# Kernel optimization log

Measured on AMD Instinct MI355X. Metric: run time of the kernel, lower is better.

Reference implementation:

```python
import jax, jax.numpy as jnp
import numpy as np

N_NODES = 50000
N_EDGES = 500000
D_IN = 128
D_OUT = 128


def setup_inputs() -> dict:
    key = jax.random.key(0)
    k1, k2, k3 = jax.random.split(key, 3)
    x = jax.random.normal(k1, (N_NODES, D_IN), dtype=jnp.float32)
    edge_index = jax.random.randint(k2, (2, N_EDGES), 0, N_NODES, dtype=jnp.int64)
    W = jax.random.normal(k3, (D_IN, D_OUT), dtype=jnp.float32) / np.sqrt(D_IN)
    b = jnp.zeros((D_OUT,), dtype=jnp.float32)
    return {"x": x, "edge_index": edge_index, "W": W, "b": b}


def reference(x, edge_index, W, b):
    # GCNConv (PyG defaults): add self-loops, symmetric normalization, linear, bias.
    N = x.shape[0]
    loop = jnp.arange(N, dtype=edge_index.dtype)
    src = jnp.concatenate([edge_index[0], loop])  # message source (row)
    dst = jnp.concatenate([edge_index[1], loop])  # aggregation target (col)
    # degree of target nodes (with self-loops)
    deg = jax.ops.segment_sum(jnp.ones_like(dst, dtype=x.dtype), dst, num_segments=N)
    dinv = jnp.where(deg > 0, jax.lax.rsqrt(deg), 0.0)
    norm = dinv[src] * dinv[dst]  # [E+N]
    xw = x @ W                    # [N, D_OUT] transform before propagate
    msg = xw[src] * norm[:, None] # [E+N, D_OUT] gather + normalize
    out = jax.ops.segment_sum(msg, dst, num_segments=N) + b
    # relu; dropout is identity at inference
    return jax.nn.relu(out)
```

## Files before the change

### kernel.cpp

```cpp
#include <hip/hip_runtime.h>

#define NN 50000
#define NE 500000
#define DD 128
#define CAP 64
#define SPILLCAP 4096

typedef __attribute__((ext_vector_type(8))) short bf16x8;
typedef __attribute__((ext_vector_type(4))) float f32x4;


__device__ __forceinline__ unsigned int bf16pair(float a, float b) {
    unsigned int ua = __float_as_uint(a);
    ua = (ua + 0x7FFFu + ((ua >> 16) & 1u)) >> 16;
    unsigned int ub = __float_as_uint(b);
    ub = (ub + 0x7FFFu + ((ub >> 16) & 1u)) >> 16;
    return ua | (ub << 16);
}
__device__ __forceinline__ float bflo(unsigned int u) { return __uint_as_float(u << 16); }
__device__ __forceinline__ float bfhi(unsigned int u) { return __uint_as_float(u & 0xFFFF0000u); }

__global__ void k_init(const float* __restrict__ W, unsigned int* __restrict__ Wf,
                       int* __restrict__ cnt, int* __restrict__ spill_n) {
    int blk = blockIdx.x, t = threadIdx.x;
    if (blk < 8) {
        int id = blk * 256 + t;
        int lane = id & 63;
        int ts = id >> 6;
        int t8 = ts >> 2, s = ts & 3;
        int col = t8 * 16 + (lane & 15);
        int k0 = s * 32 + (lane >> 4) * 8;
#pragma unroll
        for (int j = 0; j < 4; ++j) {
            float a = W[(k0 + 2 * j) * DD + col];
            float bb = W[(k0 + 2 * j + 1) * DD + col];
            Wf[id * 4 + j] = bf16pair(a, bb);
        }
    } else {
        int i = (blk - 8) * 256 + t;
        if (i < NN) cnt[i] = 0;
        if (i == NN) *spill_n = 0;
    }
}

__global__ __launch_bounds__(256) void k_hist_gemm(
    const int* __restrict__ ei, int* __restrict__ cnt, int* __restrict__ col,
    int* __restrict__ spill, int* __restrict__ spill_n,
    const float* __restrict__ x, const unsigned int* __restrict__ Wf,
    unsigned short* __restrict__ xs, int n, int e) {
    const int blk = blockIdx.x, t = threadIdx.x;
    if (blk & 1) {
        int i = (blk >> 1) * 256 + t;
        if (i >= e) return;
        bool is64 = (ei[1] == 0) & (ei[3] == 0) & (ei[5] == 0) & (ei[7] == 0);
        int s, d;
        if (is64) {
            s = ((const int2*)ei)[i].x;
            d = ((const int2*)ei)[e + i].x;
        } else {
            s = ei[i];
            d = ei[e + i];
        }
        int pos = atomicAdd(&cnt[d], 1);
        if (pos < CAP) {
            col[(size_t)d * CAP + pos] = s;
        } else {
            int sp = atomicAdd(spill_n, 1);
            if (sp < SPILLCAP) {
                spill[2 * sp] = d;
                spill[2 * sp + 1] = s;
            }
        }
        return;
    }
    const int g = blk >> 1;
    if (g >= (n + 63) / 64) return;
    const int wave = t >> 6, lane = t & 63;
    const int row0 = g * 64 + wave * 16;
    const int arow = min(row0 + (lane & 15), n - 1);
    const int kbase = (lane >> 4) * 8;

    bf16x8 af[4];
#pragma unroll
    for (int s = 0; s < 4; ++s) {
        const float* px = &x[(size_t)arow * DD + s * 32 + kbase];
        float4 a0 = *(const float4*)px;
        float4 a1 = *(const float4*)(px + 4);
        unsigned int p[4];
        p[0] = bf16pair(a0.x, a0.y);
        p[1] = bf16pair(a0.z, a0.w);
        p[2] = bf16pair(a1.x, a1.y);
        p[3] = bf16pair(a1.z, a1.w);
        af[s] = __builtin_bit_cast(bf16x8, *(f32x4*)p);
    }
    f32x4 acc[8] = {};
#pragma unroll
    for (int s = 0; s < 4; ++s) {
#pragma unroll
        for (int t8 = 0; t8 < 8; ++t8) {
            bf16x8 bf = *(const bf16x8*)&Wf[((t8 * 4 + s) * 64 + lane) * 4];
            acc[t8] = __builtin_amdgcn_mfma_f32_16x16x32_bf16(af[s], bf, acc[t8], 0, 0, 0);
        }
    }
    const int rrow0 = row0 + (lane >> 4) * 4;
    const int colb = lane & 15;
#pragma unroll
    for (int i = 0; i < 4; ++i) {
        int r = rrow0 + i;
        if (r < n) {
#pragma unroll
            for (int t8 = 0; t8 < 8; ++t8) {
                float v = acc[t8][i];
                unsigned int uv = __float_as_uint(v);
                uv = (uv + 0x7FFFu + ((uv >> 16) & 1u)) >> 16;
                xs[(size_t)r * DD + t8 * 16 + colb] = (unsigned short)uv;
            }
        }
    }
}

__global__ __launch_bounds__(256) void k_aggr(
    const int* __restrict__ cnt, const int* __restrict__ col,
    const int* __restrict__ spill, const int* __restrict__ spill_n,
    const unsigned int* __restrict__ xs, const float* __restrict__ b,
    float* __restrict__ out) {
    int wid = (blockIdx.x * blockDim.x + threadIdx.x) >> 6;
    int lane = threadIdx.x & 63;
    if (wid >= NN) return;
    int deg = cnt[wid];
    float dvd = rsqrtf((float)deg + 1.0f);
    unsigned int u = xs[(size_t)wid * 64 + lane];
    float ax = bflo(u) * dvd, ay = bfhi(u) * dvd;

    const int* myb = col + (size_t)wid * CAP;
    int nb = min(deg, CAP);
    for (int jb = 0; jb < nb; jb += 8) {
        int4 c0 = *(const int4*)&myb[jb];
        int4 c1 = *(const int4*)&myb[jb + 4];
        int sA[8] = {c0.x, c0.y, c0.z, c0.w, c1.x, c1.y, c1.z, c1.w};
        int cn[8];
        unsigned int uu[8];
#pragma unroll
        for (int k = 0; k < 8; ++k) {
            int s = (jb + k < nb) ? sA[k] : wid;
            cn[k] = cnt[s];
            uu[k] = xs[(size_t)s * 64 + lane];
        }
#pragma unroll
        for (int k = 0; k < 8; ++k) {
            float m = (jb + k < nb) ? rsqrtf((float)cn[k] + 1.0f) : 0.0f;
            ax = fmaf(bflo(uu[k]), m, ax);
            ay = fmaf(bfhi(uu[k]), m, ay);
        }
    }
    int ns = min(*spill_n, SPILLCAP);
    for (int k = 0; k < ns; ++k) {
        if (spill[2 * k] == wid) {
            int s = spill[2 * k + 1];
            float m = rsqrtf((float)cnt[s] + 1.0f);
            unsigned int us = xs[(size_t)s * 64 + lane];
            ax = fmaf(bflo(us), m, ax);
            ay = fmaf(bfhi(us), m, ay);
        }
    }
    float2 bb = *(const float2*)&b[lane * 2];
    float ox = fmaxf(fmaf(ax, dvd, bb.x), 0.f);
    float oy = fmaxf(fmaf(ay, dvd, bb.y), 0.f);
    *(float2*)&out[(size_t)wid * DD + lane * 2] = make_float2(ox, oy);
}

extern "C" void kernel_launch(void* const* d_in, const int* in_sizes, int n_in,
                              void* d_out, int out_size, void* d_ws, size_t ws_size,
                              hipStream_t stream) {
    const float* x  = (const float*)d_in[0];
    const int*   ei = (const int*)d_in[1];
    const float* W  = (const float*)d_in[2];
    const float* b  = (const float*)d_in[3];
    float* out = (float*)d_out;

    char* p = (char*)d_ws;
    unsigned short* xs      = (unsigned short*)p; p += (size_t)NN * DD * sizeof(unsigned short);
    int*            colW    = (int*)p;            p += (size_t)NN * CAP * sizeof(int);
    int*            cnt     = (int*)p;            p += NN * sizeof(int);
    int*            spill   = (int*)p;            p += 2 * SPILLCAP * sizeof(int);
    int*            spill_n = (int*)p;            p += sizeof(int);
    unsigned int*   Wf      = (unsigned int*)p;   p += 2048 * 4 * sizeof(unsigned int);

    const int nb_e = (NE + 255) / 256;

    k_init<<<8 + (NN + 1 + 255) / 256, 256, 0, stream>>>(W, Wf, cnt, spill_n);
    k_hist_gemm<<<2 * nb_e, 256, 0, stream>>>(ei, cnt, colW, spill, spill_n,
                                              x, Wf, xs, NN, NE);
    k_aggr<<<(NN * 64 + 255) / 256, 256, 0, stream>>>(cnt, colW, spill, spill_n,
                                                      (const unsigned int*)xs, b, out);
}
```

Before: 65.95 us.

## Store adjacency as 16-bit indices, compact the fused grid, unroll gathers by 16

Neighbor indices in the bucketed adjacency are now stored as 16-bit values, since the node count fits in 16 bits. This halves the bytes written during bucketing and read during aggregation. The fused histogram/GEMM launch now places all GEMM tiles first and edge blocks after, instead of interleaving, which removes the many empty blocks that previously exited at once. The aggregation loop now processes 16 neighbors per iteration to keep more gathers in flight, at the cost of more padded dummy loads for low-degree nodes and higher register use.

```diff
diff --git a/kernel.cpp b/kernel.cpp
--- a/kernel.cpp
+++ b/kernel.cpp
@@ -5,6 +5,7 @@
 #define DD 128
 #define CAP 64
 #define SPILLCAP 4096
+#define NTILE ((NN + 63) / 64)
 
 typedef __attribute__((ext_vector_type(8))) short bf16x8;
 typedef __attribute__((ext_vector_type(4))) float f32x4;
@@ -44,13 +45,14 @@
 }
 
 __global__ __launch_bounds__(256) void k_hist_gemm(
-    const int* __restrict__ ei, int* __restrict__ cnt, int* __restrict__ col,
+    const int* __restrict__ ei, int* __restrict__ cnt,
+    unsigned short* __restrict__ col,
     int* __restrict__ spill, int* __restrict__ spill_n,
     const float* __restrict__ x, const unsigned int* __restrict__ Wf,
     unsigned short* __restrict__ xs, int n, int e) {
     const int blk = blockIdx.x, t = threadIdx.x;
-    if (blk & 1) {
-        int i = (blk >> 1) * 256 + t;
+    if (blk >= NTILE) {
+        int i = (blk - NTILE) * 256 + t;
         if (i >= e) return;
         bool is64 = (ei[1] == 0) & (ei[3] == 0) & (ei[5] == 0) & (ei[7] == 0);
         int s, d;
@@ -63,7 +65,7 @@
         }
         int pos = atomicAdd(&cnt[d], 1);
         if (pos < CAP) {
-            col[(size_t)d * CAP + pos] = s;
+            col[(size_t)d * CAP + pos] = (unsigned short)s;
         } else {
             int sp = atomicAdd(spill_n, 1);
             if (sp < SPILLCAP) {
@@ -73,8 +75,7 @@
         }
         return;
     }
-    const int g = blk >> 1;
-    if (g >= (n + 63) / 64) return;
+    const int g = blk;
     const int wave = t >> 6, lane = t & 63;
     const int row0 = g * 64 + wave * 16;
     const int arow = min(row0 + (lane & 15), n - 1);
@@ -120,7 +121,7 @@
 }
 
 __global__ __launch_bounds__(256) void k_aggr(
-    const int* __restrict__ cnt, const int* __restrict__ col,
+    const int* __restrict__ cnt, const unsigned short* __restrict__ col,
     const int* __restrict__ spill, const int* __restrict__ spill_n,
     const unsigned int* __restrict__ xs, const float* __restrict__ b,
     float* __restrict__ out) {
@@ -132,22 +133,23 @@
     unsigned int u = xs[(size_t)wid * 64 + lane];
     float ax = bflo(u) * dvd, ay = bfhi(u) * dvd;
 
-    const int* myb = col + (size_t)wid * CAP;
+    const unsigned short* myb = col + (size_t)wid * CAP;
     int nb = min(deg, CAP);
-    for (int jb = 0; jb < nb; jb += 8) {
-        int4 c0 = *(const int4*)&myb[jb];
-        int4 c1 = *(const int4*)&myb[jb + 4];
-        int sA[8] = {c0.x, c0.y, c0.z, c0.w, c1.x, c1.y, c1.z, c1.w};
-        int cn[8];
-        unsigned int uu[8];
+    for (int jb = 0; jb < nb; jb += 16) {
+        uint4 c0 = *(const uint4*)&myb[jb];
+        uint4 c1 = *(const uint4*)&myb[jb + 8];
+        unsigned int w[8] = {c0.x, c0.y, c0.z, c0.w, c1.x, c1.y, c1.z, c1.w};
+        int cn[16];
+        unsigned int uu[16];
 #pragma unroll
-        for (int k = 0; k < 8; ++k) {
-            int s = (jb + k < nb) ? sA[k] : wid;
+        for (int k = 0; k < 16; ++k) {
+            int sk = (k & 1) ? (int)(w[k >> 1] >> 16) : (int)(w[k >> 1] & 0xFFFFu);
+            int s = (jb + k < nb) ? sk : wid;
             cn[k] = cnt[s];
             uu[k] = xs[(size_t)s * 64 + lane];
         }
 #pragma unroll
-        for (int k = 0; k < 8; ++k) {
+        for (int k = 0; k < 16; ++k) {
             float m = (jb + k < nb) ? rsqrtf((float)cn[k] + 1.0f) : 0.0f;
             ax = fmaf(bflo(uu[k]), m, ax);
             ay = fmaf(bfhi(uu[k]), m, ay);
@@ -180,7 +182,7 @@
 
     char* p = (char*)d_ws;
     unsigned short* xs      = (unsigned short*)p; p += (size_t)NN * DD * sizeof(unsigned short);
-    int*            colW    = (int*)p;            p += (size_t)NN * CAP * sizeof(int);
+    unsigned short* colW    = (unsigned short*)p; p += (size_t)NN * CAP * sizeof(unsigned short);
     int*            cnt     = (int*)p;            p += NN * sizeof(int);
     int*            spill   = (int*)p;            p += 2 * SPILLCAP * sizeof(int);
     int*            spill_n = (int*)p;            p += sizeof(int);
@@ -189,8 +191,8 @@
     const int nb_e = (NE + 255) / 256;
 
     k_init<<<8 + (NN + 1 + 255) / 256, 256, 0, stream>>>(W, Wf, cnt, spill_n);
-    k_hist_gemm<<<2 * nb_e, 256, 0, stream>>>(ei, cnt, colW, spill, spill_n,
-                                              x, Wf, xs, NN, NE);
+    k_hist_gemm<<<NTILE + nb_e, 256, 0, stream>>>(ei, cnt, colW, spill, spill_n,
+                                                  x, Wf, xs, NN, NE);
     k_aggr<<<(NN * 64 + 255) / 256, 256, 0, stream>>>(cnt, colW, spill, spill_n,
                                                       (const unsigned int*)xs, b, out);
 }
```

Measured after the change: 83.97 us. 27.3% more time.
